# Kernel tuning notes

Measured on AMD Instinct MI355X. Metric: run time of the kernel, lower is better.

Reference implementation:

```python
import jax, jax.numpy as jnp
import numpy as np

N_NODES = 50000
N_EDGES = 800000
IN_DIM = 128
NUM_GRAPHS = 64
NEG_SLOPE = 0.2  # PyG GATConv default


def _gat_layer(x, src, dst, W, a_s, a_d, b):
    """PyG GATConv (concat=True), eval mode (no dropout).
    x: [N, Fin]; W: [H*C, Fin]; a_s, a_d: [H, C]; b: [H*C]."""
    N = x.shape[0]
    H, C = a_s.shape
    h = (x @ W.T).reshape(N, H, C)                      # [N,H,C]
    es = jnp.einsum('nhc,hc->nh', h, a_s)               # [N,H]
    ed = jnp.einsum('nhc,hc->nh', h, a_d)               # [N,H]
    e = jax.nn.leaky_relu(es[src] + ed[dst], NEG_SLOPE)  # [E,H]
    # segment softmax over incoming edges of each destination node
    m = jax.ops.segment_max(e, dst, num_segments=N)     # [N,H]
    ex = jnp.exp(e - m[dst])
    denom = jax.ops.segment_sum(ex, dst, num_segments=N)
    alpha = ex / denom[dst]                             # [E,H]
    out = jax.ops.segment_sum(h[src] * alpha[:, :, None], dst, num_segments=N)
    return out.reshape(N, H * C) + b


def _make_params(key):
    dims = [(512, IN_DIM, 8, 64), (256, 512, 8, 32), (128, 256, 8, 16), (512, 128, 8, 64)]
    ps = {}
    k = key
    for i, (out_f, in_f, H, C) in enumerate(dims, 1):
        k, k1, k2, k3 = jax.random.split(k, 4)
        s = 1.0 / np.sqrt(in_f)
        ps[f'W{i}'] = jax.random.normal(k1, (out_f, in_f), jnp.float32) * s
        ps[f'a{i}s'] = jax.random.normal(k2, (H, C), jnp.float32) * 0.1
        ps[f'a{i}d'] = jax.random.normal(k3, (H, C), jnp.float32) * 0.1
        ps[f'b{i}'] = jnp.zeros((out_f,), jnp.float32)
    k, k1, k2 = jax.random.split(k, 3)
    ps['lw1'] = jax.random.normal(k1, (32, 512), jnp.float32) * (1.0 / np.sqrt(512))
    ps['lb1'] = jnp.zeros((32,), jnp.float32)
    ps['lw2'] = jax.random.normal(k2, (2, 32), jnp.float32) * (1.0 / np.sqrt(32))
    ps['lb2'] = jnp.zeros((2,), jnp.float32)
    return ps


def setup_inputs() -> dict:
    key = jax.random.key(0)
    kx, ke, kb, kp = jax.random.split(key, 4)
    x = jax.random.normal(kx, (N_NODES, IN_DIM), jnp.float32)
    edge_index = jax.random.randint(ke, (2, N_EDGES), 0, N_NODES, jnp.int64 if jax.config.jax_enable_x64 else jnp.int32)
    batch = jnp.sort(jax.random.randint(kb, (N_NODES,), 0, NUM_GRAPHS, edge_index.dtype))
    inp = {'x': x, 'edge_index': edge_index, 'batch': batch}
    inp.update(_make_params(kp))
    return inp


def reference(x, edge_index, batch,
              W1, a1s, a1d, b1, W2, a2s, a2d, b2,
              W3, a3s, a3d, b3, W4, a4s, a4d, b4,
              lw1, lb1, lw2, lb2):
    N = x.shape[0]
    # PyG GATConv add_self_loops=True
    loop = jnp.arange(N, dtype=edge_index.dtype)
    src = jnp.concatenate([edge_index[0], loop])
    dst = jnp.concatenate([edge_index[1], loop])

    h = jax.nn.elu(_gat_layer(x, src, dst, W1, a1s, a1d, b1))
    h = jax.nn.elu(_gat_layer(h, src, dst, W2, a2s, a2d, b2))
    h = jax.nn.elu(_gat_layer(h, src, dst, W3, a3s, a3d, b3))
    h = _gat_layer(h, src, dst, W4, a4s, a4d, b4)

    # global mean pool over graphs
    sums = jax.ops.segment_sum(h, batch, num_segments=NUM_GRAPHS)
    cnts = jax.ops.segment_sum(jnp.ones((N, 1), h.dtype), batch, num_segments=NUM_GRAPHS)
    g = sums / jnp.maximum(cnts, 1.0)                   # [G, 512]

    g = jax.nn.elu(g @ lw1.T + lb1)                     # dropout skipped (eval)
    return g @ lw2.T + lb2                              # [G, 2]
```

## Files before the change

### kernel.cpp

```cpp
#include <hip/hip_runtime.h>
#include <math.h>

#define NN 50000
#define NE 800000
#define NEP (NE + NN)
#define NEPP 1000000
#define NGR 64
#define NHEAD 8
#define MPAD 50048
#define KSTASH 6

typedef short short8 __attribute__((ext_vector_type(8)));
typedef float floatx4 __attribute__((ext_vector_type(4)));
typedef unsigned uintx4 __attribute__((ext_vector_type(4)));

__device__ inline float bf2f(short s) {
    union { unsigned u; float f; } v;
    v.u = ((unsigned)(unsigned short)s) << 16;
    return v.f;
}
__device__ inline float bf2f_lo(unsigned p) {
    union { unsigned u; float f; } v; v.u = p << 16; return v.f;
}
__device__ inline float bf2f_hi(unsigned p) {
    union { unsigned u; float f; } v; v.u = p & 0xffff0000u; return v.f;
}
__device__ inline short f2bf(float f) {
    union { float f; unsigned u; } v; v.f = f;
    unsigned r = v.u + 0x7fffu + ((v.u >> 16) & 1u);
    return (short)(r >> 16);
}

__device__ inline void gl_lds16(const short* g, short* l) {
    __builtin_amdgcn_global_load_lds(
        (const __attribute__((address_space(1))) unsigned int*)g,
        (__attribute__((address_space(3))) unsigned int*)l, 16, 0, 0);
}

__global__ void count_deg(const int* __restrict__ ei, int* __restrict__ deg) {
    int e = blockIdx.x * 256 + threadIdx.x;
    if (e >= NEP) return;
    int d = (e < NE) ? ei[NE + e] : (e - NE);
    atomicAdd(&deg[d], 1);
}

__global__ __launch_bounds__(1024) void scan_local(const int* __restrict__ deg,
                                                   int* __restrict__ out,
                                                   int* __restrict__ bsum, int n) {
    __shared__ int sd[1024];
    int b = blockIdx.x, t = threadIdx.x;
    int i = b * 1024 + t;
    int v = (i < n) ? ((deg[i] + 3) & ~3) : 0;
    sd[t] = v;
    __syncthreads();
    for (int off = 1; off < 1024; off <<= 1) {
        int tmp = (t >= off) ? sd[t - off] : 0;
        __syncthreads();
        sd[t] += tmp;
        __syncthreads();
    }
    if (i < n) out[i] = sd[t] - v;
    if (t == 1023) bsum[b] = sd[1023];
}

__global__ void scan_bsum(int* __restrict__ bsum, int nb) {
    if (threadIdx.x == 0) {
        int s = 0;
        for (int i = 0; i < nb; i++) { int v = bsum[i]; bsum[i] = s; s += v; }
        bsum[nb] = s;
    }
}

__global__ void scan_add(int* __restrict__ row_ptr, int* __restrict__ cursor,
                         const int* __restrict__ bsum, int n, int nb) {
    int i = blockIdx.x * 256 + threadIdx.x;
    if (i < n) {
        int v = row_ptr[i] + bsum[i >> 10];
        row_ptr[i] = v;
        cursor[i] = v;
    } else if (i == n) {
        row_ptr[n] = bsum[nb];
    }
}

__global__ void scatter_edges(const int* __restrict__ ei, int* __restrict__ cursor,
                              int* __restrict__ srcs) {
    int e = blockIdx.x * 256 + threadIdx.x;
    if (e >= NEP) return;
    int s, d;
    if (e < NE) { s = ei[e]; d = ei[NE + e]; }
    else        { s = e - NE; d = e - NE; }
    int pos = atomicAdd(&cursor[d], 1);
    srcs[pos] = s;
}

__global__ void conv_w_all(const float* __restrict__ w0, const float* __restrict__ w1,
                           const float* __restrict__ w2, const float* __restrict__ w3,
                           short* __restrict__ out) {
    int i = blockIdx.x * 256 + threadIdx.x;
    if (i >= 294912) return;
    const float* src; int off;
    if (i < 65536)       { src = w0; off = i; }
    else if (i < 196608) { src = w1; off = i - 65536; }
    else if (i < 229376) { src = w2; off = i - 196608; }
    else                 { src = w3; off = i - 229376; }
    out[i] = f2bf(src[off]);
}

__global__ void conv_x_pad4(const float* __restrict__ x, short* __restrict__ xb) {
    int i = blockIdx.x * 256 + threadIdx.x;
    if (i >= MPAD * 32) return;
    int r = i >> 5;
    short4 o;
    if (r < NN) {
        float4 v = *(const float4*)&x[(size_t)i * 4];
        o.x = f2bf(v.x); o.y = f2bf(v.y); o.z = f2bf(v.z); o.w = f2bf(v.w);
    } else {
        o.x = o.y = o.z = o.w = 0;
    }
    *(short4*)&xb[(size_t)i * 4] = o;
}

template <int C>
__global__ __launch_bounds__(256) void gemm_bf(const short* __restrict__ A,
                                               const short* __restrict__ B,
                                               short* __restrict__ Cout,
                                               const float* __restrict__ a_s,
                                               const float* __restrict__ a_d,
                                               float* __restrict__ es,
                                               float* __restrict__ ed,
                                               int K) {
    constexpr int Nc = 8 * C;
    constexpr int colTiles = Nc / 128;
    constexpr int JPH = C / 16;
    constexpr int HPW = 64 / C;
    __shared__ __align__(16) short As[128 * 64];
    __shared__ __align__(16) short Bs[128 * 64];
    int bx = blockIdx.x % colTiles;
    int by = blockIdx.x / colTiles;
    int row0 = by * 128, col0 = bx * 128;
    int t = threadIdx.x;
    int lane = t & 63, w = t >> 6;
    int wr = (w >> 1) * 64, wc = (w & 1) * 64;
    int lrow = lane & 15, lq = lane >> 4;

    int srow = lane >> 3;
    int kcsrc = (lane & 7) ^ srow;

    floatx4 acc[4][4];
#pragma unroll
    for (int i = 0; i < 4; i++)
#pragma unroll
        for (int j = 0; j < 4; j++) acc[i][j] = (floatx4)0.0f;

    for (int k0 = 0; k0 < K; k0 += 64) {
#pragma unroll
        for (int it = 0; it < 4; it++) {
            int r0 = w * 32 + it * 8;
            int r = r0 + srow;
            gl_lds16(&A[(size_t)(row0 + r) * K + k0 + kcsrc * 8], &As[r0 * 64]);
            gl_lds16(&B[(size_t)(col0 + r) * K + k0 + kcsrc * 8], &Bs[r0 * 64]);
        }
        __syncthreads();
#pragma unroll
        for (int kk = 0; kk < 2; kk++) {
            int slot = (kk * 4 + lq) ^ (lrow & 7);
            short8 af[4], bfr[4];
#pragma unroll
            for (int i = 0; i < 4; i++)
                af[i] = *(const short8*)&As[(wr + i * 16 + lrow) * 64 + slot * 8];
#pragma unroll
            for (int j = 0; j < 4; j++)
                bfr[j] = *(const short8*)&Bs[(wc + j * 16 + lrow) * 64 + slot * 8];
#pragma unroll
            for (int i = 0; i < 4; i++)
#pragma unroll
                for (int j = 0; j < 4; j++)
                    acc[i][j] = __builtin_amdgcn_mfma_f32_16x16x32_bf16(af[i], bfr[j], acc[i][j], 0, 0, 0);
        }
        __syncthreads();
    }

#pragma unroll
    for (int i = 0; i < 4; i++)
#pragma unroll
        for (int j = 0; j < 4; j++)
#pragma unroll
            for (int r = 0; r < 4; r++) {
                int row = row0 + wr + i * 16 + lq * 4 + r;
                int col = col0 + wc + j * 16 + lrow;
                Cout[(size_t)row * Nc + col] = f2bf(acc[i][j][r]);
            }

    float asv[4], adv[4];
#pragma unroll
    for (int j = 0; j < 4; j++) {
        int colA = col0 + wc + j * 16 + lrow;
        asv[j] = a_s[colA];
        adv[j] = a_d[colA];
    }
    int hb = (col0 + wc) / C;
#pragma unroll
    for (int i = 0; i < 4; i++)
#pragma unroll
        for (int r = 0; r < 4; r++) {
            float s_h[HPW], d_h[HPW];
#pragma unroll
            for (int hh = 0; hh < HPW; hh++) { s_h[hh] = 0.f; d_h[hh] = 0.f; }
#pragma unroll
            for (int j = 0; j < 4; j++) {
                s_h[j / JPH] = fmaf(acc[i][j][r], asv[j], s_h[j / JPH]);
                d_h[j / JPH] = fmaf(acc[i][j][r], adv[j], d_h[j / JPH]);
            }
#pragma unroll
            for (int hh = 0; hh < HPW; hh++) {
#pragma unroll
                for (int off = 1; off <= 8; off <<= 1) {
                    s_h[hh] += __shfl_xor(s_h[hh], off);
                    d_h[hh] += __shfl_xor(d_h[hh], off);
                }
            }
            if (lrow == 0) {
                int row = row0 + wr + i * 16 + lq * 4 + r;
                if (row < NN) {
#pragma unroll
                    for (int hh = 0; hh < HPW; hh++) {
                        es[row * 8 + hb + hh] = s_h[hh];
                        ed[row * 8 + hb + hh] = d_h[hh];
                    }
                }
            }
        }
}

__global__ __launch_bounds__(256) void alpha_kernel(const float* __restrict__ es,
                                                    const float* __restrict__ ed,
                                                    const int* __restrict__ row_ptr,
                                                    const int* __restrict__ degr,
                                                    const int* __restrict__ srcs,
                                                    float* __restrict__ alpha) {
    int wave = threadIdx.x >> 6, lane = threadIdx.x & 63;
    int n = __builtin_amdgcn_readfirstlane(blockIdx.x * 4 + wave);
    int start = row_ptr[n];
    int degp = row_ptr[n + 1] - start;
    int deg = degr[n];
    int m8 = deg * 8;
    int mp8 = degp * 8;
    const int* sp = srcs + start;
    int hh = lane & 7;
    float edv = ed[n * 8 + hh];
    float st[KSTASH];
    float pm = -1e30f, ps = 0.f;
#pragma unroll
    for (int i = 0; i < KSTASH; i++) {
        int idx = lane + i * 64;
        if (idx < m8) {
            int s = sp[idx >> 3];
            float e = es[s * 8 + hh] + edv;
            e = e > 0.f ? e : 0.2f * e;
            st[i] = e;
            float mn = fmaxf(pm, e);
            ps = ps * __expf(pm - mn) + __expf(e - mn);
            pm = mn;
        }
    }
    for (int idx = lane + KSTASH * 64; idx < m8; idx += 64) {
        int s = sp[idx >> 3];
        float e = es[s * 8 + hh] + edv;
        e = e > 0.f ? e : 0.2f * e;
        float mn = fmaxf(pm, e);
        ps = ps * __expf(pm - mn) + __expf(e - mn);
        pm = mn;
    }
#pragma unroll
    for (int off = 8; off <= 32; off <<= 1) {
        float mo = __shfl_xor(pm, off);
        float so = __shfl_xor(ps, off);
        float mn = fmaxf(pm, mo);
        ps = ps * __expf(pm - mn) + so * __expf(mo - mn);
        pm = mn;
    }
    float invd = 1.0f / ps;
    int hoff = hh * NEPP;
#pragma unroll
    for (int i = 0; i < KSTASH; i++) {
        int idx = lane + i * 64;
        if (idx < m8) alpha[hoff + start + (idx >> 3)] = __expf(st[i] - pm) * invd;
    }
    for (int idx = lane + KSTASH * 64; idx < m8; idx += 64) {
        int s = sp[idx >> 3];
        float e = es[s * 8 + hh] + edv;
        e = e > 0.f ? e : 0.2f * e;
        alpha[hoff + start + (idx >> 3)] = __expf(e - pm) * invd;
    }
    for (int idx = m8 + lane; idx < mp8; idx += 64)
        alpha[(size_t)(idx & 7) * NEPP + start + (idx >> 3)] = 0.f;
}

template <int C, bool ELU>
__global__ __launch_bounds__(256) void aggr_npg(const short* __restrict__ h,
                                                const float* __restrict__ alpha,
                                                const int* __restrict__ row_ptr,
                                                const int* __restrict__ srcs,
                                                const float* __restrict__ bias,
                                                short* __restrict__ out) {
    constexpr int HC = NHEAD * C;
    constexpr int NCH = HC / 64;
    constexpr int RSH = (C == 64) ? 10 : (C == 32) ? 9 : 8;
    int chunk = blockIdx.x % NCH;
    int grp   = blockIdx.x / NCH;
    int lane = threadIdx.x & 63;
    int wave = threadIdx.x >> 6;
    int sub = lane & 7;
    int g   = lane >> 3;
    int n = grp * 32 + wave * 8 + g;
    int c0 = chunk * 64 + sub * 8;
    unsigned c02 = (unsigned)(c0 * 2);
    int head = c0 / C;
    bool valid = n < NN;
    int start = 0, degp = 0;
    if (valid) {
        start = row_ptr[n];
        degp = row_ptr[n + 1] - start;
    }
    unsigned soff = (unsigned)start;
    unsigned aoff = (unsigned)(head * NEPP + start);
    float acc[8];
#pragma unroll
    for (int j = 0; j < 8; j++) acc[j] = 0.f;
    for (int k = 0; k < degp; k += 4) {
        int s0 = srcs[soff + k];
        int s1 = srcs[soff + k + 1];
        int s2 = srcs[soff + k + 2];
        int s3 = srcs[soff + k + 3];
        float w0 = alpha[aoff + k];
        float w1 = alpha[aoff + k + 1];
        float w2 = alpha[aoff + k + 2];
        float w3 = alpha[aoff + k + 3];
        uintx4 h0 = *(const uintx4*)((const char*)h + (((unsigned)s0 << RSH) + c02));
        uintx4 h1 = *(const uintx4*)((const char*)h + (((unsigned)s1 << RSH) + c02));
        uintx4 h2 = *(const uintx4*)((const char*)h + (((unsigned)s2 << RSH) + c02));
        uintx4 h3 = *(const uintx4*)((const char*)h + (((unsigned)s3 << RSH) + c02));
#pragma unroll
        for (int j = 0; j < 4; j++) {
            acc[2 * j]     = fmaf(w0, bf2f_lo(h0[j]), acc[2 * j]);
            acc[2 * j + 1] = fmaf(w0, bf2f_hi(h0[j]), acc[2 * j + 1]);
        }
#pragma unroll
        for (int j = 0; j < 4; j++) {
            acc[2 * j]     = fmaf(w1, bf2f_lo(h1[j]), acc[2 * j]);
            acc[2 * j + 1] = fmaf(w1, bf2f_hi(h1[j]), acc[2 * j + 1]);
        }
#pragma unroll
        for (int j = 0; j < 4; j++) {
            acc[2 * j]     = fmaf(w2, bf2f_lo(h2[j]), acc[2 * j]);
            acc[2 * j + 1] = fmaf(w2, bf2f_hi(h2[j]), acc[2 * j + 1]);
        }
#pragma unroll
        for (int j = 0; j < 4; j++) {
            acc[2 * j]     = fmaf(w3, bf2f_lo(h3[j]), acc[2 * j]);
            acc[2 * j + 1] = fmaf(w3, bf2f_hi(h3[j]), acc[2 * j + 1]);
        }
    }
    if (valid) {
        floatx4 b0 = *(const floatx4*)&bias[c0];
        floatx4 b1 = *(const floatx4*)&bias[c0 + 4];
        float bb[8] = {b0[0], b0[1], b0[2], b0[3], b1[0], b1[1], b1[2], b1[3]};
        unsigned pk[4];
#pragma unroll
        for (int j = 0; j < 4; j++) {
            float o0 = acc[2 * j] + bb[2 * j];
            float o1 = acc[2 * j + 1] + bb[2 * j + 1];
            if (ELU) {
                o0 = o0 > 0.f ? o0 : (__expf(o0) - 1.0f);
                o1 = o1 > 0.f ? o1 : (__expf(o1) - 1.0f);
            }
            pk[j] = ((unsigned)(unsigned short)f2bf(o0)) |
                    (((unsigned)(unsigned short)f2bf(o1)) << 16);
        }
        *(uintx4*)&out[(size_t)n * HC + c0] = *(uintx4*)pk;
    }
}

__global__ __launch_bounds__(256) void pool_kernel(const short* __restrict__ h,
                                                   const int* __restrict__ batch,
                                                   float* __restrict__ gout) {
    __shared__ float red[4 * 64];
    int g = blockIdx.x >> 3;
    int fc = (blockIdx.x & 7) * 64;
    int lo = 0, hi = NN;
    while (lo < hi) { int mid = (lo + hi) >> 1; if (batch[mid] < g) lo = mid + 1; else hi = mid; }
    int s = lo;
    lo = 0; hi = NN;
    while (lo < hi) { int mid = (lo + hi) >> 1; if (batch[mid] < g + 1) lo = mid + 1; else hi = mid; }
    int e = lo;
    int t = threadIdx.x;
    int wave = t >> 6, lane = t & 63;
    int f8 = (lane & 7) * 8;
    int stripe = wave * 8 + (lane >> 3);
    float acc[8];
#pragma unroll
    for (int j = 0; j < 8; j++) acc[j] = 0.f;
    for (int r = s + stripe; r < e; r += 32) {
        short8 v = *(const short8*)&h[(size_t)r * 512 + fc + f8];
#pragma unroll
        for (int j = 0; j < 8; j++) acc[j] += bf2f(v[j]);
    }
#pragma unroll
    for (int j = 0; j < 8; j++) {
        acc[j] += __shfl_xor(acc[j], 8);
        acc[j] += __shfl_xor(acc[j], 16);
        acc[j] += __shfl_xor(acc[j], 32);
    }
    if (lane < 8) {
#pragma unroll
        for (int j = 0; j < 8; j++) red[wave * 64 + lane * 8 + j] = acc[j];
    }
    __syncthreads();
    if (t < 64) {
        float v = red[t] + red[64 + t] + red[128 + t] + red[192 + t];
        float inv = 1.0f / fmaxf((float)(e - s), 1.0f);
        gout[g * 512 + fc + t] = v * inv;
    }
}

__global__ __launch_bounds__(64) void mlp_kernel(const float* __restrict__ g,
                                                 const float* __restrict__ lw1,
                                                 const float* __restrict__ lb1,
                                                 const float* __restrict__ lw2,
                                                 const float* __restrict__ lb2,
                                                 float* __restrict__ outp) {
    __shared__ float gv[512];
    __shared__ float y1[32];
    int b = blockIdx.x, t = threadIdx.x;
    for (int i = t; i < 512; i += 64) gv[i] = g[b * 512 + i];
    __syncthreads();
    if (t < 32) {
        float a = lb1[t];
        for (int k = 0; k < 512; k++) a = fmaf(gv[k], lw1[t * 512 + k], a);
        y1[t] = a > 0.f ? a : (__expf(a) - 1.0f);
    }
    __syncthreads();
    if (t < 2) {
        float a = lb2[t];
        for (int k = 0; k < 32; k++) a = fmaf(y1[k], lw2[t * 32 + k], a);
        outp[b * 2 + t] = a;
    }
}

extern "C" void kernel_launch(void* const* d_in, const int* in_sizes, int n_in,
                              void* d_out, int out_size, void* d_ws, size_t ws_size,
                              hipStream_t stream) {
    (void)in_sizes; (void)n_in; (void)out_size; (void)ws_size;
    const float* x     = (const float*)d_in[0];
    const int*   ei    = (const int*)d_in[1];
    const int*   batch = (const int*)d_in[2];
    const float* W[4]  = {(const float*)d_in[3], (const float*)d_in[7],
                          (const float*)d_in[11], (const float*)d_in[15]};
    const float* As_[4] = {(const float*)d_in[4], (const float*)d_in[8],
                           (const float*)d_in[12], (const float*)d_in[16]};
    const float* Ad_[4] = {(const float*)d_in[5], (const float*)d_in[9],
                           (const float*)d_in[13], (const float*)d_in[17]};
    const float* Bi[4]  = {(const float*)d_in[6], (const float*)d_in[10],
                           (const float*)d_in[14], (const float*)d_in[18]};
    const float* lw1 = (const float*)d_in[19];
    const float* lb1 = (const float*)d_in[20];
    const float* lw2 = (const float*)d_in[21];
    const float* lb2 = (const float*)d_in[22];
    float* out = (float*)d_out;

    short* Ab = (short*)d_ws;
    short* Hb = Ab + (size_t)MPAD * 512;
    short* Wb = Hb + (size_t)MPAD * 512;
    short* Wb_[4] = {Wb, Wb + 65536, Wb + 196608, Wb + 229376};
    float* esb  = (float*)(Wb + 294912);
    float* edb  = esb + NN * NHEAD;
    float* gbuf = edb + NN * NHEAD;
    int* row_ptr = (int*)(gbuf + NGR * 512);
    int* cursor  = row_ptr + (NN + 1);
    int* degr    = cursor + (NN + 1);
    int* srcs    = degr + NN;
    int* bsum    = srcs + NEPP;
    float* alphab = (float*)(bsum + 64);

    const int nblk = (NN + 1023) / 1024;

    hipMemsetAsync(degr, 0, NN * sizeof(int), stream);
    count_deg<<<(NEP + 255) / 256, 256, 0, stream>>>(ei, degr);
    scan_local<<<nblk, 1024, 0, stream>>>(degr, row_ptr, bsum, NN);
    scan_bsum<<<1, 64, 0, stream>>>(bsum, nblk);
    scan_add<<<(NN + 256) / 256, 256, 0, stream>>>(row_ptr, cursor, bsum, NN, nblk);
    hipMemsetAsync(srcs, 0, NEPP * sizeof(int), stream);
    scatter_edges<<<(NEP + 255) / 256, 256, 0, stream>>>(ei, cursor, srcs);

    conv_x_pad4<<<(MPAD * 32 + 255) / 256, 256, 0, stream>>>(x, Ab);
    conv_w_all<<<(294912 + 255) / 256, 256, 0, stream>>>(W[0], W[1], W[2], W[3], Wb);

    const int rowTiles = MPAD / 128;
    const int ag  = NN / 4;
    const int ngb = (NN + 31) / 32;

    gemm_bf<64><<<rowTiles * 4, 256, 0, stream>>>(Ab, Wb_[0], Hb, As_[0], Ad_[0], esb, edb, 128);
    alpha_kernel<<<ag, 256, 0, stream>>>(esb, edb, row_ptr, degr, srcs, alphab);
    aggr_npg<64, true><<<ngb * 8, 256, 0, stream>>>(Hb, alphab, row_ptr, srcs, Bi[0], Ab);

    gemm_bf<32><<<rowTiles * 2, 256, 0, stream>>>(Ab, Wb_[1], Hb, As_[1], Ad_[1], esb, edb, 512);
    alpha_kernel<<<ag, 256, 0, stream>>>(esb, edb, row_ptr, degr, srcs, alphab);
    aggr_npg<32, true><<<ngb * 4, 256, 0, stream>>>(Hb, alphab, row_ptr, srcs, Bi[1], Ab);

    gemm_bf<16><<<rowTiles * 1, 256, 0, stream>>>(Ab, Wb_[2], Hb, As_[2], Ad_[2], esb, edb, 256);
    alpha_kernel<<<ag, 256, 0, stream>>>(esb, edb, row_ptr, degr, srcs, alphab);
    aggr_npg<16, true><<<ngb * 2, 256, 0, stream>>>(Hb, alphab, row_ptr, srcs, Bi[2], Ab);

    gemm_bf<64><<<rowTiles * 4, 256, 0, stream>>>(Ab, Wb_[3], Hb, As_[3], Ad_[3], esb, edb, 128);
    alpha_kernel<<<ag, 256, 0, stream>>>(esb, edb, row_ptr, degr, srcs, alphab);
    aggr_npg<64, false><<<ngb * 8, 256, 0, stream>>>(Hb, alphab, row_ptr, srcs, Bi[3], Ab);

    pool_kernel<<<NGR * 8, 256, 0, stream>>>(Ab, batch, gbuf);
    mlp_kernel<<<NGR, 64, 0, stream>>>(gbuf, lw1, lb1, lw2, lb2, out);
}
```

Before: 761.5 us.

## Interleave alpha by head in 8-edge blocks, vectorize aggregation loads, sort adjacency

Changes the alpha storage from head-major planes to blocks of 8 edges × 8 heads per node, with per-node padding raised to a multiple of 8 and the srcs buffer aligned so the aggregation loop can fetch four source indices and four weights as single 16-byte vector loads. Adds a per-node insertion sort of neighbor lists so gathers of h rows go in ascending address order, which may improve cache locality. The aim is fewer scalar loads in the aggregation kernels. The trade-offs are a larger padded edge buffer, more zero-fill in alpha_kernel, and an extra serial sort kernel whose cost per thread grows with the square of node degree.

```diff
diff --git a/kernel.cpp b/kernel.cpp
--- a/kernel.cpp
+++ b/kernel.cpp
@@ -4,7 +4,7 @@
 #define NN 50000
 #define NE 800000
 #define NEP (NE + NN)
-#define NEPP 1000000
+#define NEPP 1200000
 #define NGR 64
 #define NHEAD 8
 #define MPAD 50048
@@ -50,7 +50,7 @@
     __shared__ int sd[1024];
     int b = blockIdx.x, t = threadIdx.x;
     int i = b * 1024 + t;
-    int v = (i < n) ? ((deg[i] + 3) & ~3) : 0;
+    int v = (i < n) ? ((deg[i] + 7) & ~7) : 0;
     sd[t] = v;
     __syncthreads();
     for (int off = 1; off < 1024; off <<= 1) {
@@ -92,6 +92,19 @@
     else        { s = e - NE; d = e - NE; }
     int pos = atomicAdd(&cursor[d], 1);
     srcs[pos] = s;
+}
+
+__global__ void sort_adj(const int* __restrict__ row_ptr,
+                         const int* __restrict__ degr, int* __restrict__ srcs) {
+    int n = blockIdx.x * 256 + threadIdx.x;
+    if (n >= NN) return;
+    int s = row_ptr[n], d = degr[n];
+    for (int i = 1; i < d; i++) {
+        int v = srcs[s + i];
+        int j = i - 1;
+        while (j >= 0 && srcs[s + j] > v) { srcs[s + j + 1] = srcs[s + j]; j--; }
+        srcs[s + j + 1] = v;
+    }
 }
 
 __global__ void conv_w_all(const float* __restrict__ w0, const float* __restrict__ w1,
@@ -247,8 +260,10 @@
     int m8 = deg * 8;
     int mp8 = degp * 8;
     const int* sp = srcs + start;
+    float* ap = alpha + (size_t)start * 8;
     int hh = lane & 7;
     float edv = ed[n * 8 + hh];
+    int slot = ((lane & 7) << 3) | (lane >> 3);
     float st[KSTASH];
     float pm = -1e30f, ps = 0.f;
 #pragma unroll
@@ -281,20 +296,21 @@
         pm = mn;
     }
     float invd = 1.0f / ps;
-    int hoff = hh * NEPP;
 #pragma unroll
     for (int i = 0; i < KSTASH; i++) {
         int idx = lane + i * 64;
-        if (idx < m8) alpha[hoff + start + (idx >> 3)] = __expf(st[i] - pm) * invd;
+        if (idx < m8) ap[i * 64 + slot] = __expf(st[i] - pm) * invd;
     }
     for (int idx = lane + KSTASH * 64; idx < m8; idx += 64) {
         int s = sp[idx >> 3];
         float e = es[s * 8 + hh] + edv;
         e = e > 0.f ? e : 0.2f * e;
-        alpha[hoff + start + (idx >> 3)] = __expf(e - pm) * invd;
-    }
-    for (int idx = m8 + lane; idx < mp8; idx += 64)
-        alpha[(size_t)(idx & 7) * NEPP + start + (idx >> 3)] = 0.f;
+        ap[(idx >> 6) * 64 + slot] = __expf(e - pm) * invd;
+    }
+    for (int idx = m8 + lane; idx < mp8; idx += 64) {
+        int k = idx >> 3, h = idx & 7;
+        ap[(k >> 3) * 64 + h * 8 + (k & 7)] = 0.f;
+    }
 }
 
 template <int C, bool ELU>
@@ -323,43 +339,38 @@
         start = row_ptr[n];
         degp = row_ptr[n + 1] - start;
     }
-    unsigned soff = (unsigned)start;
-    unsigned aoff = (unsigned)(head * NEPP + start);
+    const int* sp = srcs + start;
+    const float* ab = alpha + (size_t)start * 8 + head * 8;
     float acc[8];
 #pragma unroll
     for (int j = 0; j < 8; j++) acc[j] = 0.f;
     for (int k = 0; k < degp; k += 4) {
-        int s0 = srcs[soff + k];
-        int s1 = srcs[soff + k + 1];
-        int s2 = srcs[soff + k + 2];
-        int s3 = srcs[soff + k + 3];
-        float w0 = alpha[aoff + k];
-        float w1 = alpha[aoff + k + 1];
-        float w2 = alpha[aoff + k + 2];
-        float w3 = alpha[aoff + k + 3];
-        uintx4 h0 = *(const uintx4*)((const char*)h + (((unsigned)s0 << RSH) + c02));
-        uintx4 h1 = *(const uintx4*)((const char*)h + (((unsigned)s1 << RSH) + c02));
-        uintx4 h2 = *(const uintx4*)((const char*)h + (((unsigned)s2 << RSH) + c02));
-        uintx4 h3 = *(const uintx4*)((const char*)h + (((unsigned)s3 << RSH) + c02));
+        int4 sv = *(const int4*)(sp + k);
+        int aoff = ((k >> 3) << 6) | (k & 4);
+        floatx4 wv = *(const floatx4*)(ab + aoff);
+        uintx4 h0 = *(const uintx4*)((const char*)h + (((unsigned)sv.x << RSH) + c02));
+        uintx4 h1 = *(const uintx4*)((const char*)h + (((unsigned)sv.y << RSH) + c02));
+        uintx4 h2 = *(const uintx4*)((const char*)h + (((unsigned)sv.z << RSH) + c02));
+        uintx4 h3 = *(const uintx4*)((const char*)h + (((unsigned)sv.w << RSH) + c02));
 #pragma unroll
         for (int j = 0; j < 4; j++) {
-            acc[2 * j]     = fmaf(w0, bf2f_lo(h0[j]), acc[2 * j]);
-            acc[2 * j + 1] = fmaf(w0, bf2f_hi(h0[j]), acc[2 * j + 1]);
+            acc[2 * j]     = fmaf(wv[0], bf2f_lo(h0[j]), acc[2 * j]);
+            acc[2 * j + 1] = fmaf(wv[0], bf2f_hi(h0[j]), acc[2 * j + 1]);
         }
 #pragma unroll
         for (int j = 0; j < 4; j++) {
-            acc[2 * j]     = fmaf(w1, bf2f_lo(h1[j]), acc[2 * j]);
-            acc[2 * j + 1] = fmaf(w1, bf2f_hi(h1[j]), acc[2 * j + 1]);
+            acc[2 * j]     = fmaf(wv[1], bf2f_lo(h1[j]), acc[2 * j]);
+            acc[2 * j + 1] = fmaf(wv[1], bf2f_hi(h1[j]), acc[2 * j + 1]);
         }
 #pragma unroll
         for (int j = 0; j < 4; j++) {
-            acc[2 * j]     = fmaf(w2, bf2f_lo(h2[j]), acc[2 * j]);
-            acc[2 * j + 1] = fmaf(w2, bf2f_hi(h2[j]), acc[2 * j + 1]);
+            acc[2 * j]     = fmaf(wv[2], bf2f_lo(h2[j]), acc[2 * j]);
+            acc[2 * j + 1] = fmaf(wv[2], bf2f_hi(h2[j]), acc[2 * j + 1]);
         }
 #pragma unroll
         for (int j = 0; j < 4; j++) {
-            acc[2 * j]     = fmaf(w3, bf2f_lo(h3[j]), acc[2 * j]);
-            acc[2 * j + 1] = fmaf(w3, bf2f_hi(h3[j]), acc[2 * j + 1]);
+            acc[2 * j]     = fmaf(wv[3], bf2f_lo(h3[j]), acc[2 * j]);
+            acc[2 * j + 1] = fmaf(wv[3], bf2f_hi(h3[j]), acc[2 * j + 1]);
         }
     }
     if (valid) {
@@ -479,7 +490,7 @@
     int* row_ptr = (int*)(gbuf + NGR * 512);
     int* cursor  = row_ptr + (NN + 1);
     int* degr    = cursor + (NN + 1);
-    int* srcs    = degr + NN;
+    int* srcs    = degr + NN + 2;
     int* bsum    = srcs + NEPP;
     float* alphab = (float*)(bsum + 64);
 
@@ -492,6 +503,7 @@
     scan_add<<<(NN + 256) / 256, 256, 0, stream>>>(row_ptr, cursor, bsum, NN, nblk);
     hipMemsetAsync(srcs, 0, NEPP * sizeof(int), stream);
     scatter_edges<<<(NEP + 255) / 256, 256, 0, stream>>>(ei, cursor, srcs);
+    sort_adj<<<(NN + 255) / 256, 256, 0, stream>>>(row_ptr, degr, srcs);
 
     conv_x_pad4<<<(MPAD * 32 + 255) / 256, 256, 0, stream>>>(x, Ab);
     conv_w_all<<<(294912 + 255) / 256, 256, 0, stream>>>(W[0], W[1], W[2], W[3], Wb);
```

New measurement: 894.0 us. 17.4% more time.

## Recompute attention weights in aggregation instead of materializing alpha array

Applied to the files above, without the earlier changes.

The alpha kernel becomes a stats kernel that only stores the per-node, per-head softmax max and reciprocal denominator. The aggregation kernel recomputes each edge weight from es, ed and these stats, so the per-edge alpha array is no longer written and read back (about 8 floats per edge). The cost is an extra gather of es per edge plus exp work, repeated by every channel chunk of the aggregation (up to 8 chunks for C=64). Padded edges beyond the real degree are masked by comparing against degr.

```diff
diff --git a/kernel.cpp b/kernel.cpp
--- a/kernel.cpp
+++ b/kernel.cpp
@@ -8,7 +8,6 @@
 #define NGR 64
 #define NHEAD 8
 #define MPAD 50048
-#define KSTASH 6
 
 typedef short short8 __attribute__((ext_vector_type(8)));
 typedef float floatx4 __attribute__((ext_vector_type(4)));
@@ -233,38 +232,23 @@
         }
 }
 
-__global__ __launch_bounds__(256) void alpha_kernel(const float* __restrict__ es,
+__global__ __launch_bounds__(256) void stats_kernel(const float* __restrict__ es,
                                                     const float* __restrict__ ed,
                                                     const int* __restrict__ row_ptr,
                                                     const int* __restrict__ degr,
                                                     const int* __restrict__ srcs,
-                                                    float* __restrict__ alpha) {
+                                                    float* __restrict__ mbuf,
+                                                    float* __restrict__ ibuf) {
     int wave = threadIdx.x >> 6, lane = threadIdx.x & 63;
     int n = __builtin_amdgcn_readfirstlane(blockIdx.x * 4 + wave);
     int start = row_ptr[n];
-    int degp = row_ptr[n + 1] - start;
     int deg = degr[n];
     int m8 = deg * 8;
-    int mp8 = degp * 8;
     const int* sp = srcs + start;
     int hh = lane & 7;
     float edv = ed[n * 8 + hh];
-    float st[KSTASH];
     float pm = -1e30f, ps = 0.f;
-#pragma unroll
-    for (int i = 0; i < KSTASH; i++) {
-        int idx = lane + i * 64;
-        if (idx < m8) {
-            int s = sp[idx >> 3];
-            float e = es[s * 8 + hh] + edv;
-            e = e > 0.f ? e : 0.2f * e;
-            st[i] = e;
-            float mn = fmaxf(pm, e);
-            ps = ps * __expf(pm - mn) + __expf(e - mn);
-            pm = mn;
-        }
-    }
-    for (int idx = lane + KSTASH * 64; idx < m8; idx += 64) {
+    for (int idx = lane; idx < m8; idx += 64) {
         int s = sp[idx >> 3];
         float e = es[s * 8 + hh] + edv;
         e = e > 0.f ? e : 0.2f * e;
@@ -280,27 +264,20 @@
         ps = ps * __expf(pm - mn) + so * __expf(mo - mn);
         pm = mn;
     }
-    float invd = 1.0f / ps;
-    int hoff = hh * NEPP;
-#pragma unroll
-    for (int i = 0; i < KSTASH; i++) {
-        int idx = lane + i * 64;
-        if (idx < m8) alpha[hoff + start + (idx >> 3)] = __expf(st[i] - pm) * invd;
-    }
-    for (int idx = lane + KSTASH * 64; idx < m8; idx += 64) {
-        int s = sp[idx >> 3];
-        float e = es[s * 8 + hh] + edv;
-        e = e > 0.f ? e : 0.2f * e;
-        alpha[hoff + start + (idx >> 3)] = __expf(e - pm) * invd;
-    }
-    for (int idx = m8 + lane; idx < mp8; idx += 64)
-        alpha[(size_t)(idx & 7) * NEPP + start + (idx >> 3)] = 0.f;
+    if (lane < 8) {
+        mbuf[n * 8 + lane] = pm;
+        ibuf[n * 8 + lane] = 1.0f / ps;
+    }
 }
 
 template <int C, bool ELU>
 __global__ __launch_bounds__(256) void aggr_npg(const short* __restrict__ h,
-                                                const float* __restrict__ alpha,
+                                                const float* __restrict__ es,
+                                                const float* __restrict__ ed,
+                                                const float* __restrict__ mbuf,
+                                                const float* __restrict__ ibuf,
                                                 const int* __restrict__ row_ptr,
+                                                const int* __restrict__ degr,
                                                 const int* __restrict__ srcs,
                                                 const float* __restrict__ bias,
                                                 short* __restrict__ out) {
@@ -318,13 +295,17 @@
     unsigned c02 = (unsigned)(c0 * 2);
     int head = c0 / C;
     bool valid = n < NN;
-    int start = 0, degp = 0;
+    int start = 0, degp = 0, deg = 0;
+    float mv = 0.f, iv = 0.f, edv = 0.f;
     if (valid) {
         start = row_ptr[n];
         degp = row_ptr[n + 1] - start;
+        deg = degr[n];
+        mv = mbuf[n * 8 + head];
+        iv = ibuf[n * 8 + head];
+        edv = ed[n * 8 + head];
     }
     unsigned soff = (unsigned)start;
-    unsigned aoff = (unsigned)(head * NEPP + start);
     float acc[8];
 #pragma unroll
     for (int j = 0; j < 8; j++) acc[j] = 0.f;
@@ -333,10 +314,18 @@
         int s1 = srcs[soff + k + 1];
         int s2 = srcs[soff + k + 2];
         int s3 = srcs[soff + k + 3];
-        float w0 = alpha[aoff + k];
-        float w1 = alpha[aoff + k + 1];
-        float w2 = alpha[aoff + k + 2];
-        float w3 = alpha[aoff + k + 3];
+        float e0 = es[s0 * 8 + head] + edv;
+        float e1 = es[s1 * 8 + head] + edv;
+        float e2 = es[s2 * 8 + head] + edv;
+        float e3 = es[s3 * 8 + head] + edv;
+        e0 = e0 > 0.f ? e0 : 0.2f * e0;
+        e1 = e1 > 0.f ? e1 : 0.2f * e1;
+        e2 = e2 > 0.f ? e2 : 0.2f * e2;
+        e3 = e3 > 0.f ? e3 : 0.2f * e3;
+        float w0 = (k     < deg) ? __expf(e0 - mv) * iv : 0.f;
+        float w1 = (k + 1 < deg) ? __expf(e1 - mv) * iv : 0.f;
+        float w2 = (k + 2 < deg) ? __expf(e2 - mv) * iv : 0.f;
+        float w3 = (k + 3 < deg) ? __expf(e3 - mv) * iv : 0.f;
         uintx4 h0 = *(const uintx4*)((const char*)h + (((unsigned)s0 << RSH) + c02));
         uintx4 h1 = *(const uintx4*)((const char*)h + (((unsigned)s1 << RSH) + c02));
         uintx4 h2 = *(const uintx4*)((const char*)h + (((unsigned)s2 << RSH) + c02));
@@ -475,13 +464,14 @@
     short* Wb_[4] = {Wb, Wb + 65536, Wb + 196608, Wb + 229376};
     float* esb  = (float*)(Wb + 294912);
     float* edb  = esb + NN * NHEAD;
-    float* gbuf = edb + NN * NHEAD;
+    float* mbuf = edb + NN * NHEAD;
+    float* ibuf = mbuf + NN * NHEAD;
+    float* gbuf = ibuf + NN * NHEAD;
     int* row_ptr = (int*)(gbuf + NGR * 512);
     int* cursor  = row_ptr + (NN + 1);
     int* degr    = cursor + (NN + 1);
     int* srcs    = degr + NN;
     int* bsum    = srcs + NEPP;
-    float* alphab = (float*)(bsum + 64);
 
     const int nblk = (NN + 1023) / 1024;
 
@@ -501,20 +491,20 @@
     const int ngb = (NN + 31) / 32;
 
     gemm_bf<64><<<rowTiles * 4, 256, 0, stream>>>(Ab, Wb_[0], Hb, As_[0], Ad_[0], esb, edb, 128);
-    alpha_kernel<<<ag, 256, 0, stream>>>(esb, edb, row_ptr, degr, srcs, alphab);
-    aggr_npg<64, true><<<ngb * 8, 256, 0, stream>>>(Hb, alphab, row_ptr, srcs, Bi[0], Ab);
+    stats_kernel<<<ag, 256, 0, stream>>>(esb, edb, row_ptr, degr, srcs, mbuf, ibuf);
+    aggr_npg<64, true><<<ngb * 8, 256, 0, stream>>>(Hb, esb, edb, mbuf, ibuf, row_ptr, degr, srcs, Bi[0], Ab);
 
     gemm_bf<32><<<rowTiles * 2, 256, 0, stream>>>(Ab, Wb_[1], Hb, As_[1], Ad_[1], esb, edb, 512);
-    alpha_kernel<<<ag, 256, 0, stream>>>(esb, edb, row_ptr, degr, srcs, alphab);
-    aggr_npg<32, true><<<ngb * 4, 256, 0, stream>>>(Hb, alphab, row_ptr, srcs, Bi[1], Ab);
+    stats_kernel<<<ag, 256, 0, stream>>>(esb, edb, row_ptr, degr, srcs, mbuf, ibuf);
+    aggr_npg<32, true><<<ngb * 4, 256, 0, stream>>>(Hb, esb, edb, mbuf, ibuf, row_ptr, degr, srcs, Bi[1], Ab);
 
     gemm_bf<16><<<rowTiles * 1, 256, 0, stream>>>(Ab, Wb_[2], Hb, As_[2], Ad_[2], esb, edb, 256);
-    alpha_kernel<<<ag, 256, 0, stream>>>(esb, edb, row_ptr, degr, srcs, alphab);
-    aggr_npg<16, true><<<ngb * 2, 256, 0, stream>>>(Hb, alphab, row_ptr, srcs, Bi[2], Ab);
+    stats_kernel<<<ag, 256, 0, stream>>>(esb, edb, row_ptr, degr, srcs, mbuf, ibuf);
+    aggr_npg<16, true><<<ngb * 2, 256, 0, stream>>>(Hb, esb, edb, mbuf, ibuf, row_ptr, degr, srcs, Bi[2], Ab);
 
     gemm_bf<64><<<rowTiles * 4, 256, 0, stream>>>(Ab, Wb_[3], Hb, As_[3], Ad_[3], esb, edb, 128);
-    alpha_kernel<<<ag, 256, 0, stream>>>(esb, edb, row_ptr, degr, srcs, alphab);
-    aggr_npg<64, false><<<ngb * 8, 256, 0, stream>>>(Hb, alphab, row_ptr, srcs, Bi[3], Ab);
+    stats_kernel<<<ag, 256, 0, stream>>>(esb, edb, row_ptr, degr, srcs, mbuf, ibuf);
+    aggr_npg<64, false><<<ngb * 8, 256, 0, stream>>>(Hb, esb, edb, mbuf, ibuf, row_ptr, degr, srcs, Bi[3], Ab);
 
     pool_kernel<<<NGR * 8, 256, 0, stream>>>(Ab, batch, gbuf);
     mlp_kernel<<<NGR, 64, 0, stream>>>(gbuf, lw1, lb1, lw2, lb2, out);
```

After: 836.3 us. +9.8%, slower.
